# Kernel tuning notes

Hardware: AMD Instinct MI355X
Metric: run time of the kernel (lower is better)

## Reference

```python
import jax, jax.numpy as jnp
import numpy as np

B, S, D, H = 2, 2048, 1024, 16
HD = D // H  # head dim = 64


def setup_inputs() -> dict:
    key = jax.random.key(0)
    ks = jax.random.split(key, 8)
    s = 0.02
    return {
        "Q": jax.random.normal(ks[0], (B, S, D), jnp.float32),
        "K": jax.random.normal(ks[1], (B, S, D), jnp.float32),
        "V": jax.random.normal(ks[2], (B, S, D), jnp.float32),
        "mask": jax.random.randint(ks[3], (1, 1, S, S), 0, 2, jnp.int32),
        "Wq": jax.random.normal(ks[4], (D, D), jnp.float32) * s,
        "bq": jnp.zeros((D,), jnp.float32),
        "Wk": jax.random.normal(ks[5], (D, D), jnp.float32) * s,
        "bk": jnp.zeros((D,), jnp.float32),
        "Wv": jax.random.normal(ks[6], (D, D), jnp.float32) * s,
        "bv": jnp.zeros((D,), jnp.float32),
        "Wo": jax.random.normal(ks[7], (D, D), jnp.float32) * s,
        "bo": jnp.zeros((D,), jnp.float32),
    }


def reference(Q, K, V, mask, Wq, bq, Wk, bk, Wv, bv, Wo, bo):
    b = Q.shape[0]
    # QKV projections, split into heads: [B,S,D] -> [B,H,S,HD]
    q = (Q @ Wq + bq).reshape(b, -1, H, HD).transpose(0, 2, 1, 3)
    k = (K @ Wk + bk).reshape(b, -1, H, HD).transpose(0, 2, 1, 3)
    v = (V @ Wv + bv).reshape(b, -1, H, HD).transpose(0, 2, 1, 3)
    # scaled dot-product attention with full [B,H,S,S] scores (as in source)
    scale = jnp.sqrt(jnp.asarray(HD, q.dtype))
    scores = jnp.einsum("bhqd,bhkd->bhqk", q, k) / scale
    scores = jnp.where(mask == 0, -jnp.inf, scores)
    attn = jax.nn.softmax(scores, axis=-1)
    ctx = jnp.einsum("bhqk,bhkd->bhqd", attn, v)
    # merge heads and output projection
    concat = ctx.transpose(0, 2, 1, 3).reshape(b, -1, H * HD)
    return concat @ Wo + bo
```

## Files before the change

### kernel.cpp

```cpp
#include <hip/hip_runtime.h>


using s8v = __attribute__((ext_vector_type(8))) short;
using f4v = __attribute__((ext_vector_type(4))) float;
typedef unsigned long long u64;

__device__ __forceinline__ unsigned short f2bf(float f) {
  union { float f; unsigned int u; } v; v.f = f;
  return (unsigned short)((v.u + 0x7fffu + ((v.u >> 16) & 1u)) >> 16);
}

__device__ __forceinline__ void gll16(const void* g, void* l) {
  __builtin_amdgcn_global_load_lds(
      (const __attribute__((address_space(1))) unsigned int*)g,
      (__attribute__((address_space(3))) unsigned int*)l, 16, 0, 0);
}

__global__ void f2b3_kernel(const float* __restrict__ A, const float* __restrict__ B,
                            const float* __restrict__ C, unsigned short* __restrict__ oA,
                            unsigned short* __restrict__ oB, unsigned short* __restrict__ oC) {
  int z = blockIdx.x >> 12;
  int idx = (blockIdx.x & 4095) * 256 + threadIdx.x;
  const float* in = (z == 0) ? A : (z == 1) ? B : C;
  unsigned short* out = (z == 0) ? oA : (z == 1) ? oB : oC;
  float4 v = ((const float4*)in)[idx];
  ushort4 o;
  o.x = f2bf(v.x); o.y = f2bf(v.y); o.z = f2bf(v.z); o.w = f2bf(v.w);
  ((ushort4*)out)[idx] = o;
}

__global__ void packmask_kernel(const int* __restrict__ mask, u64* __restrict__ bm) {
  int gw = (int)((blockIdx.x * 256 + threadIdx.x) >> 6);
  int lane = threadIdx.x & 63;
  int mv = mask[(size_t)gw * 64 + lane];
  u64 bal = __ballot(mv != 0);
  if (lane == 0) bm[gw] = bal;
}

__global__ void wtrans4_kernel(const float* __restrict__ W0, const float* __restrict__ W1,
                               const float* __restrict__ W2, const float* __restrict__ W3,
                               unsigned short* __restrict__ T0, unsigned short* __restrict__ T1,
                               unsigned short* __restrict__ T2, unsigned short* __restrict__ T3) {
  __shared__ unsigned short t[64][72];
  int z = blockIdx.z;
  const float* W = (z == 0) ? W0 : (z == 1) ? W1 : (z == 2) ? W2 : W3;
  unsigned short* Wt = (z == 0) ? T0 : (z == 1) ? T1 : (z == 2) ? T2 : T3;
  int k0 = blockIdx.x * 64, n0 = blockIdx.y * 64;
  int tid = threadIdx.x;
  for (int p = 0; p < 4; ++p) {
    int idx = p * 256 + tid;
    int row = idx >> 4, c4 = idx & 15;
    float4 v = *(const float4*)&W[(size_t)(k0 + row) * 1024 + n0 + c4 * 4];
    t[row][c4 * 4 + 0] = f2bf(v.x);
    t[row][c4 * 4 + 1] = f2bf(v.y);
    t[row][c4 * 4 + 2] = f2bf(v.z);
    t[row][c4 * 4 + 3] = f2bf(v.w);
  }
  __syncthreads();
  for (int p = 0; p < 2; ++p) {
    int idx = p * 256 + tid;
    int j = idx >> 3, c8 = idx & 7;
    unsigned short tmp[8];
    for (int i = 0; i < 8; ++i) tmp[i] = t[c8 * 8 + i][j];
    uint4 o;
    o.x = tmp[0] | ((unsigned)tmp[1] << 16);
    o.y = tmp[2] | ((unsigned)tmp[3] << 16);
    o.z = tmp[4] | ((unsigned)tmp[5] << 16);
    o.w = tmp[6] | ((unsigned)tmp[7] << 16);
    *(uint4*)&Wt[(size_t)(n0 + j) * 1024 + k0 + c8 * 8] = o;
  }
}

__global__ __launch_bounds__(256) void proj3_kernel(
    const unsigned short* __restrict__ A0, const unsigned short* __restrict__ A1,
    const unsigned short* __restrict__ A2,
    const unsigned short* __restrict__ W0, const unsigned short* __restrict__ W1,
    const unsigned short* __restrict__ W2,
    const float* __restrict__ b0, const float* __restrict__ b1, const float* __restrict__ b2,
    unsigned short* __restrict__ oq, unsigned short* __restrict__ ok,
    unsigned short* __restrict__ ovt) {
  const int z = blockIdx.z;
  const unsigned short* A  = (z == 0) ? A0 : (z == 1) ? A1 : A2;
  const unsigned short* Wt = (z == 0) ? W0 : (z == 1) ? W1 : W2;
  const float* bias        = (z == 0) ? b0 : (z == 1) ? b1 : b2;

  __shared__ __align__(16) unsigned short As[128 * 32];
  __shared__ __align__(16) unsigned short Bs[128 * 32];

  const int tid = threadIdx.x;
  const int lane = tid & 63, w = tid >> 6, ln = lane & 15, quad = lane >> 4;
  const int wm = (w & 1) * 64, wn = (w >> 1) * 64;
  const int m0 = blockIdx.x * 128, n0 = blockIdx.y * 128;

  const int srow = w * 32 + (lane >> 2);
  const int schunk = (lane & 3) ^ ((lane >> 2) & 3);
  const int cfrag = (quad ^ (ln & 3)) * 8;

  f4v zero = {0.f, 0.f, 0.f, 0.f};
  f4v acc[4][4];
  for (int mi = 0; mi < 4; ++mi)
    for (int ni = 0; ni < 4; ++ni) acc[mi][ni] = zero;

  for (int kt = 0; kt < 1024; kt += 32) {
    __syncthreads();
    gll16(&A[(size_t)(m0 + srow) * 1024 + kt + schunk * 8],       &As[(w * 32) * 32]);
    gll16(&A[(size_t)(m0 + srow + 16) * 1024 + kt + schunk * 8],  &As[(w * 32 + 16) * 32]);
    gll16(&Wt[(size_t)(n0 + srow) * 1024 + kt + schunk * 8],      &Bs[(w * 32) * 32]);
    gll16(&Wt[(size_t)(n0 + srow + 16) * 1024 + kt + schunk * 8], &Bs[(w * 32 + 16) * 32]);
    __syncthreads();
    s8v a[4], b[4];
    for (int mi = 0; mi < 4; ++mi) a[mi] = *(const s8v*)&As[(wm + mi * 16 + ln) * 32 + cfrag];
    for (int ni = 0; ni < 4; ++ni) b[ni] = *(const s8v*)&Bs[(wn + ni * 16 + ln) * 32 + cfrag];
    if (z < 2) {
      for (int mi = 0; mi < 4; ++mi)
        for (int ni = 0; ni < 4; ++ni)
          acc[mi][ni] = __builtin_amdgcn_mfma_f32_16x16x32_bf16(a[mi], b[ni], acc[mi][ni], 0, 0, 0);
    } else {
      for (int mi = 0; mi < 4; ++mi)
        for (int ni = 0; ni < 4; ++ni)
          acc[mi][ni] = __builtin_amdgcn_mfma_f32_16x16x32_bf16(b[ni], a[mi], acc[mi][ni], 0, 0, 0);
    }
  }

  if (z < 2) {
    const float qscale = (z == 0) ? 0.18033688f : 1.0f;
    unsigned short* outp = (z == 0) ? oq : ok;
    for (int mi = 0; mi < 4; ++mi) {
      int rb = m0 + wm + mi * 16 + quad * 4;
      int b_ = rb >> 11;
      for (int ni = 0; ni < 4; ++ni) {
        int col = n0 + wn + ni * 16 + ln;
        float bvv = bias[col];
        int h = col >> 6, hd = col & 63;
        size_t ob = (size_t)(b_ * 16 + h) * 2048;
        for (int r = 0; r < 4; ++r) {
          int s = (rb + r) & 2047;
          outp[(ob + s) * 64 + hd] = f2bf((acc[mi][ni][r] + bvv) * qscale);
        }
      }
    }
  } else {
    for (int ni = 0; ni < 4; ++ni) {
      for (int r = 0; r < 4; ++r) {
        int colw = n0 + wn + ni * 16 + quad * 4 + r;
        int h = colw >> 6, hd = colw & 63;
        float bvv = bias[colw];
        for (int mi = 0; mi < 4; ++mi) {
          int sg = m0 + wm + mi * 16 + ln;
          int b_ = sg >> 11, ss = sg & 2047;
          ovt[((size_t)(b_ * 16 + h) * 64 + hd) * 2048 + ss] = f2bf(acc[mi][ni][r] + bvv);
        }
      }
    }
  }
}

__global__ __launch_bounds__(256) void flash_kernel(
    const unsigned short* __restrict__ q, const unsigned short* __restrict__ k,
    const unsigned short* __restrict__ vt, const u64* __restrict__ bm,
    unsigned short* __restrict__ ctx) {
  __shared__ __align__(16) unsigned short qp_s[128][72];
  __shared__ __align__(16) unsigned short k_s[64][72];
  __shared__ __align__(16) unsigned short v_s[80][72];

  const int tid = threadIdx.x;
  const int lane = tid & 63, w = tid >> 6, ln = lane & 15, quad = lane >> 4;
  const int q0 = blockIdx.x * 128;
  const int bh = blockIdx.y;
  const unsigned short* qg  = q  + ((size_t)bh * 2048 + q0) * 64;
  const unsigned short* kgb = k  + (size_t)bh * 2048 * 64;
  const unsigned short* vgb = vt + (size_t)bh * 64 * 2048;

  for (int j = 0; j < 5; ++j) {
    int idx = j * 256 + tid;
    if (idx < 16 * 72) ((unsigned short*)v_s[64])[idx] = 0;
  }
  for (int p = 0; p < 4; ++p) {
    int c = p * 256 + tid;
    int row = c >> 3, c8 = c & 7;
    *(uint4*)&qp_s[row][c8 * 8] = *(const uint4*)&qg[(size_t)row * 64 + c8 * 8];
  }
  __syncthreads();
  if (tid < 64) v_s[64][tid] = 0x3F80;
  __syncthreads();

  s8v aq[2][2];
  for (int s = 0; s < 2; ++s)
    for (int h = 0; h < 2; ++h)
      aq[s][h] = *(const s8v*)&qp_s[s * 64 + w * 16 + ln][h * 32 + quad * 8];
  s8v bones0 = *(const s8v*)&v_s[64 + ln][quad * 8];
  s8v bones1 = *(const s8v*)&v_s[64 + ln][32 + quad * 8];

  const int srow0 = tid >> 3, sc8 = tid & 7;
  const int srow1 = 32 + srow0;

  const u64* bmr0 = bm + (size_t)(q0 + w * 16 + ln) * 32;
  const u64* bmr1 = bmr0 + 64 * 32;

  uint4 kr0 = *(const uint4*)&kgb[(size_t)srow0 * 64 + sc8 * 8];
  uint4 kr1 = *(const uint4*)&kgb[(size_t)srow1 * 64 + sc8 * 8];
  uint4 vr0 = *(const uint4*)&vgb[(size_t)srow0 * 2048 + sc8 * 8];
  uint4 vr1 = *(const uint4*)&vgb[(size_t)srow1 * 2048 + sc8 * 8];
  u64 mwc[2], mwn[2];
  mwc[0] = bmr0[0];
  mwc[1] = bmr1[0];

  f4v zero = {0.f, 0.f, 0.f, 0.f};
  f4v l_acc[2];
  f4v o_acc[2][4];
  for (int s = 0; s < 2; ++s) {
    l_acc[s] = zero;
    for (int ni = 0; ni < 4; ++ni) o_acc[s][ni] = zero;
  }

  for (int kt = 0; kt < 2048; kt += 64) {
    *(uint4*)&k_s[srow0][sc8 * 8] = kr0;
    *(uint4*)&k_s[srow1][sc8 * 8] = kr1;
    *(uint4*)&v_s[srow0][sc8 * 8] = vr0;
    *(uint4*)&v_s[srow1][sc8 * 8] = vr1;
    if (kt + 64 < 2048) {
      int ktn = kt + 64;
      kr0 = *(const uint4*)&kgb[(size_t)(ktn + srow0) * 64 + sc8 * 8];
      kr1 = *(const uint4*)&kgb[(size_t)(ktn + srow1) * 64 + sc8 * 8];
      vr0 = *(const uint4*)&vgb[(size_t)srow0 * 2048 + ktn + sc8 * 8];
      vr1 = *(const uint4*)&vgb[(size_t)srow1 * 2048 + ktn + sc8 * 8];
      int ktcn = ktn >> 6;
      mwn[0] = bmr0[ktcn];
      mwn[1] = bmr1[ktcn];
    }
    __syncthreads();

    f4v sc[2][4];
    for (int ni = 0; ni < 4; ++ni) {
      s8v ak0 = *(const s8v*)&k_s[ni * 16 + ln][quad * 8];
      s8v ak1 = *(const s8v*)&k_s[ni * 16 + ln][32 + quad * 8];
      for (int s = 0; s < 2; ++s) {
        f4v t = zero;
        t = __builtin_amdgcn_mfma_f32_16x16x32_bf16(ak0, aq[s][0], t, 0, 0, 0);
        t = __builtin_amdgcn_mfma_f32_16x16x32_bf16(ak1, aq[s][1], t, 0, 0, 0);
        sc[s][ni] = t;
      }
    }

    for (int s = 0; s < 2; ++s) {
      u64 m = mwc[s] >> (quad * 4);
      unsigned mlo = (unsigned)m, mhi = (unsigned)(m >> 32);
      for (int ni = 0; ni < 4; ++ni) {
        unsigned msel = ((ni < 2) ? mlo : mhi) >> ((ni & 1) * 16);
        unsigned u0 = __float_as_uint(__builtin_amdgcn_exp2f(sc[s][ni][0]) * (float)(msel & 1u));
        unsigned u1 = __float_as_uint(__builtin_amdgcn_exp2f(sc[s][ni][1]) * (float)((msel >> 1) & 1u));
        unsigned u2 = __float_as_uint(__builtin_amdgcn_exp2f(sc[s][ni][2]) * (float)((msel >> 2) & 1u));
        unsigned u3 = __float_as_uint(__builtin_amdgcn_exp2f(sc[s][ni][3]) * (float)((msel >> 3) & 1u));
        unsigned plo = __builtin_amdgcn_perm(u1, u0, 0x07060302);
        unsigned phi = __builtin_amdgcn_perm(u3, u2, 0x07060302);
        *(u64*)&qp_s[s * 64 + w * 16 + ln][ni * 16 + quad * 4] = plo | ((u64)phi << 32);
      }
      mwc[s] = mwn[s];
    }

    s8v ap[2][2];
    for (int s = 0; s < 2; ++s)
      for (int h = 0; h < 2; ++h)
        ap[s][h] = *(const s8v*)&qp_s[s * 64 + w * 16 + ln][h * 32 + quad * 8];
    for (int ni = 0; ni < 4; ++ni) {
      s8v bv0 = *(const s8v*)&v_s[ni * 16 + ln][quad * 8];
      s8v bv1 = *(const s8v*)&v_s[ni * 16 + ln][32 + quad * 8];
      for (int s = 0; s < 2; ++s) {
        o_acc[s][ni] = __builtin_amdgcn_mfma_f32_16x16x32_bf16(ap[s][0], bv0, o_acc[s][ni], 0, 0, 0);
        o_acc[s][ni] = __builtin_amdgcn_mfma_f32_16x16x32_bf16(ap[s][1], bv1, o_acc[s][ni], 0, 0, 0);
      }
    }
    for (int s = 0; s < 2; ++s) {
      l_acc[s] = __builtin_amdgcn_mfma_f32_16x16x32_bf16(ap[s][0], bones0, l_acc[s], 0, 0, 0);
      l_acc[s] = __builtin_amdgcn_mfma_f32_16x16x32_bf16(ap[s][1], bones1, l_acc[s], 0, 0, 0);
    }
    __syncthreads();
  }

  int b_ = bh >> 4, h = bh & 15;
  for (int s = 0; s < 2; ++s) {
    for (int r = 0; r < 4; ++r) {
      float lr = __shfl(l_acc[s][r], quad * 16);
      float inv = 1.f / lr;
      int srow = q0 + s * 64 + w * 16 + quad * 4 + r;
      size_t base = ((size_t)b_ * 2048 + srow) * 1024 + h * 64;
      for (int ni = 0; ni < 4; ++ni)
        ctx[base + ni * 16 + ln] = f2bf(o_acc[s][ni][r] * inv);
    }
  }
}

__global__ __launch_bounds__(256) void gemm_out_kernel(
    const unsigned short* __restrict__ A, const unsigned short* __restrict__ Wt,
    const float* __restrict__ bias, float* __restrict__ out) {
  __shared__ __align__(16) unsigned short As[128 * 32];
  __shared__ __align__(16) unsigned short Bs[128 * 32];

  const int tid = threadIdx.x;
  const int lane = tid & 63, w = tid >> 6, ln = lane & 15, quad = lane >> 4;
  const int wm = (w & 1) * 64, wn = (w >> 1) * 64;
  const int m0 = blockIdx.x * 128, n0 = blockIdx.y * 128;

  const int srow = w * 32 + (lane >> 2);
  const int schunk = (lane & 3) ^ ((lane >> 2) & 3);
  const int cfrag = (quad ^ (ln & 3)) * 8;

  f4v zero = {0.f, 0.f, 0.f, 0.f};
  f4v acc[4][4];
  for (int mi = 0; mi < 4; ++mi)
    for (int ni = 0; ni < 4; ++ni) acc[mi][ni] = zero;

  for (int kt = 0; kt < 1024; kt += 32) {
    __syncthreads();
    gll16(&A[(size_t)(m0 + srow) * 1024 + kt + schunk * 8],       &As[(w * 32) * 32]);
    gll16(&A[(size_t)(m0 + srow + 16) * 1024 + kt + schunk * 8],  &As[(w * 32 + 16) * 32]);
    gll16(&Wt[(size_t)(n0 + srow) * 1024 + kt + schunk * 8],      &Bs[(w * 32) * 32]);
    gll16(&Wt[(size_t)(n0 + srow + 16) * 1024 + kt + schunk * 8], &Bs[(w * 32 + 16) * 32]);
    __syncthreads();
    s8v a[4], b[4];
    for (int mi = 0; mi < 4; ++mi) a[mi] = *(const s8v*)&As[(wm + mi * 16 + ln) * 32 + cfrag];
    for (int ni = 0; ni < 4; ++ni) b[ni] = *(const s8v*)&Bs[(wn + ni * 16 + ln) * 32 + cfrag];
    for (int mi = 0; mi < 4; ++mi)
      for (int ni = 0; ni < 4; ++ni)
        acc[mi][ni] = __builtin_amdgcn_mfma_f32_16x16x32_bf16(a[mi], b[ni], acc[mi][ni], 0, 0, 0);
  }

  for (int mi = 0; mi < 4; ++mi) {
    int rb = m0 + wm + mi * 16 + quad * 4;
    for (int ni = 0; ni < 4; ++ni) {
      int col = n0 + wn + ni * 16 + ln;
      float bvv = bias[col];
      for (int r = 0; r < 4; ++r)
        out[(size_t)(rb + r) * 1024 + col] = acc[mi][ni][r] + bvv;
    }
  }
}

extern "C" void kernel_launch(void* const* d_in, const int* in_sizes, int n_in,
                              void* d_out, int out_size, void* d_ws, size_t ws_size,
                              hipStream_t stream) {
  const float* Q  = (const float*)d_in[0];
  const float* K  = (const float*)d_in[1];
  const float* V  = (const float*)d_in[2];
  const int* mask = (const int*)d_in[3];
  const float* Wq = (const float*)d_in[4];
  const float* bq = (const float*)d_in[5];
  const float* Wk = (const float*)d_in[6];
  const float* bk = (const float*)d_in[7];
  const float* Wv = (const float*)d_in[8];
  const float* bv = (const float*)d_in[9];
  const float* Wo = (const float*)d_in[10];
  const float* bo = (const float*)d_in[11];
  float* out = (float*)d_out;

  char* ws = (char*)d_ws;
  const size_t MB = 1u << 20;
  unsigned short* qb  = (unsigned short*)(ws + 0 * MB);
  unsigned short* kb  = (unsigned short*)(ws + 8 * MB);
  unsigned short* vb  = (unsigned short*)(ws + 16 * MB);
  unsigned short* wqt = (unsigned short*)(ws + 24 * MB);
  unsigned short* wkt = (unsigned short*)(ws + 26 * MB);
  unsigned short* wvt = (unsigned short*)(ws + 28 * MB);
  unsigned short* wot = (unsigned short*)(ws + 30 * MB);
  unsigned short* qh  = (unsigned short*)(ws + 32 * MB);
  unsigned short* kh  = (unsigned short*)(ws + 40 * MB);
  unsigned short* vth = (unsigned short*)(ws + 48 * MB);
  unsigned short* ctx = (unsigned short*)(ws + 56 * MB);
  u64* bm = (u64*)(ws + 0 * MB);

  f2b3_kernel<<<12288, 256, 0, stream>>>(Q, K, V, qb, kb, vb);
  wtrans4_kernel<<<dim3(16, 16, 4), 256, 0, stream>>>(Wq, Wk, Wv, Wo, wqt, wkt, wvt, wot);
  proj3_kernel<<<dim3(32, 8, 3), 256, 0, stream>>>(qb, kb, vb, wqt, wkt, wvt,
                                                   bq, bk, bv, qh, kh, vth);
  packmask_kernel<<<16384, 256, 0, stream>>>(mask, bm);
  flash_kernel<<<dim3(16, 32), 256, 0, stream>>>(qh, kh, vth, bm, ctx);
  gemm_out_kernel<<<dim3(32, 8), 256, 0, stream>>>(ctx, wot, bo, out);
}
```

Before: 272.3 us.

## Merge prep kernels into one launch and halve GEMM M-tile

After: 260.8 us. 4.2% less time.

```diff
diff --git a/kernel.cpp b/kernel.cpp
--- a/kernel.cpp
+++ b/kernel.cpp
@@ -16,58 +16,61 @@
       (__attribute__((address_space(3))) unsigned int*)l, 16, 0, 0);
 }
 
-__global__ void f2b3_kernel(const float* __restrict__ A, const float* __restrict__ B,
-                            const float* __restrict__ C, unsigned short* __restrict__ oA,
-                            unsigned short* __restrict__ oB, unsigned short* __restrict__ oC) {
-  int z = blockIdx.x >> 12;
-  int idx = (blockIdx.x & 4095) * 256 + threadIdx.x;
-  const float* in = (z == 0) ? A : (z == 1) ? B : C;
-  unsigned short* out = (z == 0) ? oA : (z == 1) ? oB : oC;
-  float4 v = ((const float4*)in)[idx];
-  ushort4 o;
-  o.x = f2bf(v.x); o.y = f2bf(v.y); o.z = f2bf(v.z); o.w = f2bf(v.w);
-  ((ushort4*)out)[idx] = o;
-}
-
-__global__ void packmask_kernel(const int* __restrict__ mask, u64* __restrict__ bm) {
-  int gw = (int)((blockIdx.x * 256 + threadIdx.x) >> 6);
-  int lane = threadIdx.x & 63;
-  int mv = mask[(size_t)gw * 64 + lane];
-  u64 bal = __ballot(mv != 0);
-  if (lane == 0) bm[gw] = bal;
-}
-
-__global__ void wtrans4_kernel(const float* __restrict__ W0, const float* __restrict__ W1,
-                               const float* __restrict__ W2, const float* __restrict__ W3,
-                               unsigned short* __restrict__ T0, unsigned short* __restrict__ T1,
-                               unsigned short* __restrict__ T2, unsigned short* __restrict__ T3) {
+__global__ void prep_kernel(const float* __restrict__ Q, const float* __restrict__ K,
+                            const float* __restrict__ V,
+                            unsigned short* __restrict__ qb, unsigned short* __restrict__ kb,
+                            unsigned short* __restrict__ vb,
+                            const float* __restrict__ W0, const float* __restrict__ W1,
+                            const float* __restrict__ W2, const float* __restrict__ W3,
+                            unsigned short* __restrict__ T0, unsigned short* __restrict__ T1,
+                            unsigned short* __restrict__ T2, unsigned short* __restrict__ T3,
+                            const int* __restrict__ mask, u64* __restrict__ bm) {
   __shared__ unsigned short t[64][72];
-  int z = blockIdx.z;
-  const float* W = (z == 0) ? W0 : (z == 1) ? W1 : (z == 2) ? W2 : W3;
-  unsigned short* Wt = (z == 0) ? T0 : (z == 1) ? T1 : (z == 2) ? T2 : T3;
-  int k0 = blockIdx.x * 64, n0 = blockIdx.y * 64;
-  int tid = threadIdx.x;
-  for (int p = 0; p < 4; ++p) {
-    int idx = p * 256 + tid;
-    int row = idx >> 4, c4 = idx & 15;
-    float4 v = *(const float4*)&W[(size_t)(k0 + row) * 1024 + n0 + c4 * 4];
-    t[row][c4 * 4 + 0] = f2bf(v.x);
-    t[row][c4 * 4 + 1] = f2bf(v.y);
-    t[row][c4 * 4 + 2] = f2bf(v.z);
-    t[row][c4 * 4 + 3] = f2bf(v.w);
-  }
-  __syncthreads();
-  for (int p = 0; p < 2; ++p) {
-    int idx = p * 256 + tid;
-    int j = idx >> 3, c8 = idx & 7;
-    unsigned short tmp[8];
-    for (int i = 0; i < 8; ++i) tmp[i] = t[c8 * 8 + i][j];
-    uint4 o;
-    o.x = tmp[0] | ((unsigned)tmp[1] << 16);
-    o.y = tmp[2] | ((unsigned)tmp[3] << 16);
-    o.z = tmp[4] | ((unsigned)tmp[5] << 16);
-    o.w = tmp[6] | ((unsigned)tmp[7] << 16);
-    *(uint4*)&Wt[(size_t)(n0 + j) * 1024 + k0 + c8 * 8] = o;
+  const int bid = blockIdx.x, tid = threadIdx.x;
+  if (bid < 12288) {
+    int z = bid >> 12;
+    int idx = (bid & 4095) * 256 + tid;
+    const float* in = (z == 0) ? Q : (z == 1) ? K : V;
+    unsigned short* out = (z == 0) ? qb : (z == 1) ? kb : vb;
+    float4 v = ((const float4*)in)[idx];
+    ushort4 o;
+    o.x = f2bf(v.x); o.y = f2bf(v.y); o.z = f2bf(v.z); o.w = f2bf(v.w);
+    ((ushort4*)out)[idx] = o;
+  } else if (bid < 13312) {
+    int b = bid - 12288;
+    int z = b >> 8, rem = b & 255;
+    int k0 = (rem >> 4) * 64, n0 = (rem & 15) * 64;
+    const float* W = (z == 0) ? W0 : (z == 1) ? W1 : (z == 2) ? W2 : W3;
+    unsigned short* Wt = (z == 0) ? T0 : (z == 1) ? T1 : (z == 2) ? T2 : T3;
+    for (int p = 0; p < 4; ++p) {
+      int idx = p * 256 + tid;
+      int row = idx >> 4, c4 = idx & 15;
+      float4 v = *(const float4*)&W[(size_t)(k0 + row) * 1024 + n0 + c4 * 4];
+      t[row][c4 * 4 + 0] = f2bf(v.x);
+      t[row][c4 * 4 + 1] = f2bf(v.y);
+      t[row][c4 * 4 + 2] = f2bf(v.z);
+      t[row][c4 * 4 + 3] = f2bf(v.w);
+    }
+    __syncthreads();
+    for (int p = 0; p < 2; ++p) {
+      int idx = p * 256 + tid;
+      int j = idx >> 3, c8 = idx & 7;
+      unsigned short tmp[8];
+      for (int i = 0; i < 8; ++i) tmp[i] = t[c8 * 8 + i][j];
+      uint4 o;
+      o.x = tmp[0] | ((unsigned)tmp[1] << 16);
+      o.y = tmp[2] | ((unsigned)tmp[3] << 16);
+      o.z = tmp[4] | ((unsigned)tmp[5] << 16);
+      o.w = tmp[6] | ((unsigned)tmp[7] << 16);
+      *(uint4*)&Wt[(size_t)(n0 + j) * 1024 + k0 + c8 * 8] = o;
+    }
+  } else {
+    int b = bid - 13312;
+    int gw = (b * 256 + tid) >> 6;
+    int lane = tid & 63;
+    int mv = mask[(size_t)gw * 64 + lane];
+    u64 bal = __ballot(mv != 0);
+    if (lane == 0) bm[gw] = bal;
   }
 }
 
@@ -84,39 +87,38 @@
   const unsigned short* Wt = (z == 0) ? W0 : (z == 1) ? W1 : W2;
   const float* bias        = (z == 0) ? b0 : (z == 1) ? b1 : b2;
 
-  __shared__ __align__(16) unsigned short As[128 * 32];
+  __shared__ __align__(16) unsigned short As[64 * 32];
   __shared__ __align__(16) unsigned short Bs[128 * 32];
 
   const int tid = threadIdx.x;
   const int lane = tid & 63, w = tid >> 6, ln = lane & 15, quad = lane >> 4;
-  const int wm = (w & 1) * 64, wn = (w >> 1) * 64;
-  const int m0 = blockIdx.x * 128, n0 = blockIdx.y * 128;
-
-  const int srow = w * 32 + (lane >> 2);
-  const int schunk = (lane & 3) ^ ((lane >> 2) & 3);
-  const int cfrag = (quad ^ (ln & 3)) * 8;
+  const int wm = (w & 1) * 32, wn = (w >> 1) * 64;
+  const int m0 = blockIdx.x * 64, n0 = blockIdx.y * 128;
+
+  const int slr = lane >> 2;
+  const int schunk = (lane & 3) ^ ((lane >> 3) & 3);
+  const int cfrag = (quad ^ ((ln >> 1) & 3)) * 8;
 
   f4v zero = {0.f, 0.f, 0.f, 0.f};
-  f4v acc[4][4];
-  for (int mi = 0; mi < 4; ++mi)
+  f4v acc[2][4];
+  for (int mi = 0; mi < 2; ++mi)
     for (int ni = 0; ni < 4; ++ni) acc[mi][ni] = zero;
 
   for (int kt = 0; kt < 1024; kt += 32) {
     __syncthreads();
-    gll16(&A[(size_t)(m0 + srow) * 1024 + kt + schunk * 8],       &As[(w * 32) * 32]);
-    gll16(&A[(size_t)(m0 + srow + 16) * 1024 + kt + schunk * 8],  &As[(w * 32 + 16) * 32]);
-    gll16(&Wt[(size_t)(n0 + srow) * 1024 + kt + schunk * 8],      &Bs[(w * 32) * 32]);
-    gll16(&Wt[(size_t)(n0 + srow + 16) * 1024 + kt + schunk * 8], &Bs[(w * 32 + 16) * 32]);
-    __syncthreads();
-    s8v a[4], b[4];
-    for (int mi = 0; mi < 4; ++mi) a[mi] = *(const s8v*)&As[(wm + mi * 16 + ln) * 32 + cfrag];
+    gll16(&A[(size_t)(m0 + w * 16 + slr) * 1024 + kt + schunk * 8],        &As[(w * 16) * 32]);
+    gll16(&Wt[(size_t)(n0 + w * 32 + slr) * 1024 + kt + schunk * 8],       &Bs[(w * 32) * 32]);
+    gll16(&Wt[(size_t)(n0 + w * 32 + 16 + slr) * 1024 + kt + schunk * 8],  &Bs[(w * 32 + 16) * 32]);
+    __syncthreads();
+    s8v a[2], b[4];
+    for (int mi = 0; mi < 2; ++mi) a[mi] = *(const s8v*)&As[(wm + mi * 16 + ln) * 32 + cfrag];
     for (int ni = 0; ni < 4; ++ni) b[ni] = *(const s8v*)&Bs[(wn + ni * 16 + ln) * 32 + cfrag];
     if (z < 2) {
-      for (int mi = 0; mi < 4; ++mi)
+      for (int mi = 0; mi < 2; ++mi)
         for (int ni = 0; ni < 4; ++ni)
           acc[mi][ni] = __builtin_amdgcn_mfma_f32_16x16x32_bf16(a[mi], b[ni], acc[mi][ni], 0, 0, 0);
     } else {
-      for (int mi = 0; mi < 4; ++mi)
+      for (int mi = 0; mi < 2; ++mi)
         for (int ni = 0; ni < 4; ++ni)
           acc[mi][ni] = __builtin_amdgcn_mfma_f32_16x16x32_bf16(b[ni], a[mi], acc[mi][ni], 0, 0, 0);
     }
@@ -125,7 +127,7 @@
   if (z < 2) {
     const float qscale = (z == 0) ? 0.18033688f : 1.0f;
     unsigned short* outp = (z == 0) ? oq : ok;
-    for (int mi = 0; mi < 4; ++mi) {
+    for (int mi = 0; mi < 2; ++mi) {
       int rb = m0 + wm + mi * 16 + quad * 4;
       int b_ = rb >> 11;
       for (int ni = 0; ni < 4; ++ni) {
@@ -145,7 +147,7 @@
         int colw = n0 + wn + ni * 16 + quad * 4 + r;
         int h = colw >> 6, hd = colw & 63;
         float bvv = bias[colw];
-        for (int mi = 0; mi < 4; ++mi) {
+        for (int mi = 0; mi < 2; ++mi) {
           int sg = m0 + wm + mi * 16 + ln;
           int b_ = sg >> 11, ss = sg & 2047;
           ovt[((size_t)(b_ * 16 + h) * 64 + hd) * 2048 + ss] = f2bf(acc[mi][ni][r] + bvv);
@@ -293,39 +295,38 @@
 __global__ __launch_bounds__(256) void gemm_out_kernel(
     const unsigned short* __restrict__ A, const unsigned short* __restrict__ Wt,
     const float* __restrict__ bias, float* __restrict__ out) {
-  __shared__ __align__(16) unsigned short As[128 * 32];
+  __shared__ __align__(16) unsigned short As[64 * 32];
   __shared__ __align__(16) unsigned short Bs[128 * 32];
 
   const int tid = threadIdx.x;
   const int lane = tid & 63, w = tid >> 6, ln = lane & 15, quad = lane >> 4;
-  const int wm = (w & 1) * 64, wn = (w >> 1) * 64;
-  const int m0 = blockIdx.x * 128, n0 = blockIdx.y * 128;
-
-  const int srow = w * 32 + (lane >> 2);
-  const int schunk = (lane & 3) ^ ((lane >> 2) & 3);
-  const int cfrag = (quad ^ (ln & 3)) * 8;
+  const int wm = (w & 1) * 32, wn = (w >> 1) * 64;
+  const int m0 = blockIdx.x * 64, n0 = blockIdx.y * 128;
+
+  const int slr = lane >> 2;
+  const int schunk = (lane & 3) ^ ((lane >> 3) & 3);
+  const int cfrag = (quad ^ ((ln >> 1) & 3)) * 8;
 
   f4v zero = {0.f, 0.f, 0.f, 0.f};
-  f4v acc[4][4];
-  for (int mi = 0; mi < 4; ++mi)
+  f4v acc[2][4];
+  for (int mi = 0; mi < 2; ++mi)
     for (int ni = 0; ni < 4; ++ni) acc[mi][ni] = zero;
 
   for (int kt = 0; kt < 1024; kt += 32) {
     __syncthreads();
-    gll16(&A[(size_t)(m0 + srow) * 1024 + kt + schunk * 8],       &As[(w * 32) * 32]);
-    gll16(&A[(size_t)(m0 + srow + 16) * 1024 + kt + schunk * 8],  &As[(w * 32 + 16) * 32]);
-    gll16(&Wt[(size_t)(n0 + srow) * 1024 + kt + schunk * 8],      &Bs[(w * 32) * 32]);
-    gll16(&Wt[(size_t)(n0 + srow + 16) * 1024 + kt + schunk * 8], &Bs[(w * 32 + 16) * 32]);
-    __syncthreads();
-    s8v a[4], b[4];
-    for (int mi = 0; mi < 4; ++mi) a[mi] = *(const s8v*)&As[(wm + mi * 16 + ln) * 32 + cfrag];
+    gll16(&A[(size_t)(m0 + w * 16 + slr) * 1024 + kt + schunk * 8],        &As[(w * 16) * 32]);
+    gll16(&Wt[(size_t)(n0 + w * 32 + slr) * 1024 + kt + schunk * 8],       &Bs[(w * 32) * 32]);
+    gll16(&Wt[(size_t)(n0 + w * 32 + 16 + slr) * 1024 + kt + schunk * 8],  &Bs[(w * 32 + 16) * 32]);
+    __syncthreads();
+    s8v a[2], b[4];
+    for (int mi = 0; mi < 2; ++mi) a[mi] = *(const s8v*)&As[(wm + mi * 16 + ln) * 32 + cfrag];
     for (int ni = 0; ni < 4; ++ni) b[ni] = *(const s8v*)&Bs[(wn + ni * 16 + ln) * 32 + cfrag];
-    for (int mi = 0; mi < 4; ++mi)
+    for (int mi = 0; mi < 2; ++mi)
       for (int ni = 0; ni < 4; ++ni)
         acc[mi][ni] = __builtin_amdgcn_mfma_f32_16x16x32_bf16(a[mi], b[ni], acc[mi][ni], 0, 0, 0);
   }
 
-  for (int mi = 0; mi < 4; ++mi) {
+  for (int mi = 0; mi < 2; ++mi) {
     int rb = m0 + wm + mi * 16 + quad * 4;
     for (int ni = 0; ni < 4; ++ni) {
       int col = n0 + wn + ni * 16 + ln;
@@ -365,14 +366,14 @@
   unsigned short* qh  = (unsigned short*)(ws + 32 * MB);
   unsigned short* kh  = (unsigned short*)(ws + 40 * MB);
   unsigned short* vth = (unsigned short*)(ws + 48 * MB);
-  unsigned short* ctx = (unsigned short*)(ws + 56 * MB);
-  u64* bm = (u64*)(ws + 0 * MB);
-
-  f2b3_kernel<<<12288, 256, 0, stream>>>(Q, K, V, qb, kb, vb);
-  wtrans4_kernel<<<dim3(16, 16, 4), 256, 0, stream>>>(Wq, Wk, Wv, Wo, wqt, wkt, wvt, wot);
-  proj3_kernel<<<dim3(32, 8, 3), 256, 0, stream>>>(qb, kb, vb, wqt, wkt, wvt,
+  u64* bm             = (u64*)(ws + 56 * MB);
+  unsigned short* ctx = (unsigned short*)(ws + 16 * MB);
+
+  prep_kernel<<<29696, 256, 0, stream>>>(Q, K, V, qb, kb, vb,
+                                         Wq, Wk, Wv, Wo, wqt, wkt, wvt, wot,
+                                         mask, bm);
+  proj3_kernel<<<dim3(64, 8, 3), 256, 0, stream>>>(qb, kb, vb, wqt, wkt, wvt,
                                                    bq, bk, bv, qh, kh, vth);
-  packmask_kernel<<<16384, 256, 0, stream>>>(mask, bm);
   flash_kernel<<<dim3(16, 32), 256, 0, stream>>>(qh, kh, vth, bm, ctx);
-  gemm_out_kernel<<<dim3(32, 8), 256, 0, stream>>>(ctx, wot, bo, out);
-}
+  gemm_out_kernel<<<dim3(64, 8), 256, 0, stream>>>(ctx, wot, bo, out);
+}
```
